# Performance work log

Hardware: AMD Instinct MI355X
Metric: run time of the kernel (lower is better)

Reference implementation:

```python
import jax, jax.numpy as jnp
import numpy as np

HEADS = 6
HSP = 8   # window height (idx=0, split_size=[8,8])
WSP = 8   # window width


def setup_inputs() -> dict:
    key = jax.random.key(0)
    k1, k2, k3 = jax.random.split(key, 3)
    B, C, H, W = 8, 192, 192, 192
    nw = (H // HSP) * (W // WSP)  # 576 windows per image
    kv = jax.random.normal(k1, (2, B, C, H, W), dtype=jnp.float32)
    q = jax.random.normal(k2, (B, C, H, W), dtype=jnp.float32)
    mask = jax.random.normal(k3, (nw, HSP * WSP, HSP * WSP), dtype=jnp.float32)
    return {"kv": kv, "q": q, "mask": mask}


def _vid2win(x, u, v):
    # 'b (d c) (u h) (v w) -> (b u v) d (h w) c'
    B, C, H, W = x.shape
    c = C // HEADS
    hsp, wsp = H // u, W // v
    x = x.reshape(B, HEADS, c, u, hsp, v, wsp)
    x = x.transpose(0, 3, 5, 1, 4, 6, 2)  # B,u,v,d,h,w,c
    return x.reshape(B * u * v, HEADS, hsp * wsp, c)


def reference(kv, q, mask):
    k, v = kv[0], kv[1]
    B, C, H, W = k.shape
    u, w_ = H // HSP, W // WSP
    c = C // HEADS
    scale = c ** (-0.5)
    N = HSP * WSP

    qw = _vid2win(q, u, w_)  # (B*u*w, heads, N, c)
    kw = _vid2win(k, u, w_)
    vw = _vid2win(v, u, w_)

    attn = jnp.einsum('wdnc,wdmc->wdnm', qw, kw) * scale  # (B*u*w, heads, N, N)
    # mask add: 'b (u v) d h w' + mask[None, :, None]
    attn = attn.reshape(B, u * w_, HEADS, N, N) + mask[None, :, None]
    attn = jax.nn.softmax(attn, axis=-1).reshape(B * u * w_, HEADS, N, N)

    x = jnp.einsum('wdnm,wdmc->wdnc', attn, vw)  # (B*u*w, heads, N, c)
    # '(b u v) d (h w) c -> b (d c) (u h) (v w)'
    x = x.reshape(B, u, w_, HEADS, HSP, WSP, c)
    x = x.transpose(0, 3, 6, 1, 4, 2, 5)  # B,d,c,u,h,v,w
    return x.reshape(B, C, H, W)
```

## Files before the change

### kernel.cpp

```cpp
#include <hip/hip_runtime.h>

#define HW_    36864
#define WID_   192
#define CHW_   7077888
#define VOFF_  56623104
#define SCALE_ 0.17677669529663687f

typedef short short8 __attribute__((ext_vector_type(8)));
typedef float f32x4 __attribute__((ext_vector_type(4)));

union Frag { short8 s; unsigned u[4]; };

__device__ __forceinline__ unsigned f2bf_u(float f) {
  union { float f; unsigned u; } x; x.f = f;
  return (x.u + 0x8000u) >> 16;
}
__device__ __forceinline__ unsigned pack_bf(float lo, float hi) {
  union { float f; unsigned u; } a, b; a.f = lo; b.f = hi;
  return ((a.u + 0x8000u) >> 16) | (((b.u + 0x8000u) & 0xFFFF0000u));
}

extern "C" __global__ __launch_bounds__(256, 3)
void win_attn(const float* __restrict__ kv, const float* __restrict__ q,
              const float* __restrict__ mask, float* __restrict__ out) {
  const int tid  = threadIdx.x;
  const int wid  = tid >> 6;
  const int lane = tid & 63;
  const int task = blockIdx.x * 4 + wid;
  const int d    = task % 6;
  const int widx = task / 6;
  const int b    = widx / 576;
  const int uv   = widx % 576;
  const int ui   = uv / 24;
  const int vi   = uv % 24;
  const int base = b * CHW_ + d * (32 * HW_) + ui * (8 * WID_) + vi * 8;

  const float* qg = q  + base;
  const float* kg = kv + base;
  const float* vg = kv + VOFF_ + base;
  const float* mg = mask + uv * 4096;
  float*       og = out + base;

  __shared__ unsigned smem[4][3232];
  unsigned* qsd = smem[wid];
  unsigned* ksd = qsd + 1088;
  unsigned* vtd = qsd + 2176;
  unsigned short* Ps = (unsigned short*)qsd;
  unsigned* Pd = qsd;

  {
    const int n  = lane;
    const int ro = ((n >> 3) * WID_) + (n & 7);
    #pragma unroll
    for (int c2 = 0; c2 < 16; ++c2) {
      const int ch = c2 * 2;
      const float q0 = qg[ch * HW_ + ro];
      const float q1 = qg[(ch + 1) * HW_ + ro];
      const float k0 = kg[ch * HW_ + ro];
      const float k1 = kg[(ch + 1) * HW_ + ro];
      qsd[n * 17 + c2] = pack_bf(q0, q1);
      ksd[n * 17 + c2] = pack_bf(k0, k1);
    }
  }
  {
    const int half = lane >> 5;
    const int m0   = (lane & 31) * 2;
    const int ro   = ((m0 >> 3) * WID_) + (m0 & 7);
    #pragma unroll
    for (int c2 = 0; c2 < 16; ++c2) {
      const int ch = c2 * 2 + half;
      const float2 f2 = *reinterpret_cast<const float2*>(vg + ch * HW_ + ro);
      vtd[ch * 33 + (m0 >> 1)] = pack_bf(f2.x, f2.y);
    }
  }
  __syncthreads();

  const int quad = lane >> 4;
  const int l15  = lane & 15;

  Frag qf[4], kf[4];
  #pragma unroll
  for (int t = 0; t < 4; ++t) {
    const int ad = (t * 16 + l15) * 17 + quad * 4;
    #pragma unroll
    for (int r = 0; r < 4; ++r) { qf[t].u[r] = qsd[ad + r]; kf[t].u[r] = ksd[ad + r]; }
  }

  f32x4 acc[4][4];
  #pragma unroll
  for (int tn = 0; tn < 4; ++tn)
    #pragma unroll
    for (int tm = 0; tm < 4; ++tm) {
      f32x4 z = {0.f, 0.f, 0.f, 0.f};
      acc[tn][tm] = __builtin_amdgcn_mfma_f32_16x16x32_bf16(qf[tn].s, kf[tm].s, z, 0, 0, 0);
    }

  #pragma unroll
  for (int tn = 0; tn < 4; ++tn) {
    #pragma unroll
    for (int r = 0; r < 4; ++r) {
      const int row = tn * 16 + quad * 4 + r;
      const float* mrow = mg + row * 64 + l15;
      const float e0 = __expf(fmaf(acc[tn][0][r], SCALE_, mrow[0]));
      const float e1 = __expf(fmaf(acc[tn][1][r], SCALE_, mrow[16]));
      const float e2 = __expf(fmaf(acc[tn][2][r], SCALE_, mrow[32]));
      const float e3 = __expf(fmaf(acc[tn][3][r], SCALE_, mrow[48]));
      float s = (e0 + e1) + (e2 + e3);
      s += __shfl_xor(s, 1);
      s += __shfl_xor(s, 2);
      s += __shfl_xor(s, 4);
      s += __shfl_xor(s, 8);
      const float rv = __fdividef(1.0f, s);
      const int pb = row * 66 + l15;
      Ps[pb]      = (unsigned short)f2bf_u(e0 * rv);
      Ps[pb + 16] = (unsigned short)f2bf_u(e1 * rv);
      Ps[pb + 32] = (unsigned short)f2bf_u(e2 * rv);
      Ps[pb + 48] = (unsigned short)f2bf_u(e3 * rv);
    }
  }
  __syncthreads();

  Frag va[2][2], pf[4][2];
  #pragma unroll
  for (int ct = 0; ct < 2; ++ct)
    #pragma unroll
    for (int kk = 0; kk < 2; ++kk) {
      const int ad = (ct * 16 + l15) * 33 + kk * 16 + quad * 4;
      #pragma unroll
      for (int r = 0; r < 4; ++r) va[ct][kk].u[r] = vtd[ad + r];
    }
  #pragma unroll
  for (int nt = 0; nt < 4; ++nt)
    #pragma unroll
    for (int kk = 0; kk < 2; ++kk) {
      const int ad = (nt * 16 + l15) * 33 + kk * 16 + quad * 4;
      #pragma unroll
      for (int r = 0; r < 4; ++r) pf[nt][kk].u[r] = Pd[ad + r];
    }

  #pragma unroll
  for (int ct = 0; ct < 2; ++ct)
    #pragma unroll
    for (int nt = 0; nt < 4; ++nt) {
      f32x4 z = {0.f, 0.f, 0.f, 0.f};
      f32x4 o = __builtin_amdgcn_mfma_f32_16x16x32_bf16(va[ct][0].s, pf[nt][0].s, z, 0, 0, 0);
      o       = __builtin_amdgcn_mfma_f32_16x16x32_bf16(va[ct][1].s, pf[nt][1].s, o, 0, 0, 0);
      const int n  = nt * 16 + l15;
      const int so = ((n >> 3) * WID_) + (n & 7);
      #pragma unroll
      for (int r = 0; r < 4; ++r) {
        const int ch = ct * 16 + quad * 4 + r;
        og[ch * HW_ + so] = o[r];
      }
    }
}

extern "C" void kernel_launch(void* const* d_in, const int* in_sizes, int n_in,
                              void* d_out, int out_size, void* d_ws, size_t ws_size,
                              hipStream_t stream) {
  const float* kv   = (const float*)d_in[0];
  const float* q    = (const float*)d_in[1];
  const float* mask = (const float*)d_in[2];
  win_attn<<<dim3(6912), dim3(256), 0, stream>>>(kv, q, mask, (float*)d_out);
}
```

Baseline: 1.015 ms.

## Load Q/K/V fragments directly from global, defer softmax normalization, remap blocks

Drops the LDS staging of Q, K and V: each lane now loads its MFMA fragment straight from global memory (V as float4 vectors), which removes a shared-memory round trip and both __syncthreads. The unnormalized exponentials are written to LDS, and the row reciprocal is applied to the PV output, which also lets the output be stored as f32x4 vectors after the operands are swapped. Blocks are remapped so that four adjacent windows of one (batch, head) sit in one block, shared memory shrinks, and the occupancy hint rises to 4. The direct loads are less coalesced per instruction, and rounding the unnormalized exponentials to bf16 before normalization slightly changes numerics.

After: 889.6 us. -12.4%, faster.

```diff
diff --git a/kernel.cpp b/kernel.cpp
--- a/kernel.cpp
+++ b/kernel.cpp
@@ -17,22 +17,24 @@
 }
 __device__ __forceinline__ unsigned pack_bf(float lo, float hi) {
   union { float f; unsigned u; } a, b; a.f = lo; b.f = hi;
-  return ((a.u + 0x8000u) >> 16) | (((b.u + 0x8000u) & 0xFFFF0000u));
+  return ((a.u + 0x8000u) >> 16) | ((b.u + 0x8000u) & 0xFFFF0000u);
 }
 
-extern "C" __global__ __launch_bounds__(256, 3)
+extern "C" __global__ __launch_bounds__(256, 4)
 void win_attn(const float* __restrict__ kv, const float* __restrict__ q,
               const float* __restrict__ mask, float* __restrict__ out) {
   const int tid  = threadIdx.x;
   const int wid  = tid >> 6;
   const int lane = tid & 63;
-  const int task = blockIdx.x * 4 + wid;
-  const int d    = task % 6;
-  const int widx = task / 6;
-  const int b    = widx / 576;
-  const int uv   = widx % 576;
-  const int ui   = uv / 24;
-  const int vi   = uv % 24;
+  const int bid = blockIdx.x;
+  const int bd  = bid % 48;
+  const int b   = bd / 6;
+  const int d   = bd % 6;
+  const int grp = bid / 48;
+  const int ui  = grp / 6;
+  const int vig = grp % 6;
+  const int vi  = vig * 4 + wid;
+  const int uv  = ui * 24 + vi;
   const int base = b * CHW_ + d * (32 * HW_) + ui * (8 * WID_) + vi * 8;
 
   const float* qg = q  + base;
@@ -41,39 +43,9 @@
   const float* mg = mask + uv * 4096;
   float*       og = out + base;
 
-  __shared__ unsigned smem[4][3232];
-  unsigned* qsd = smem[wid];
-  unsigned* ksd = qsd + 1088;
-  unsigned* vtd = qsd + 2176;
-  unsigned short* Ps = (unsigned short*)qsd;
-  unsigned* Pd = qsd;
-
-  {
-    const int n  = lane;
-    const int ro = ((n >> 3) * WID_) + (n & 7);
-    #pragma unroll
-    for (int c2 = 0; c2 < 16; ++c2) {
-      const int ch = c2 * 2;
-      const float q0 = qg[ch * HW_ + ro];
-      const float q1 = qg[(ch + 1) * HW_ + ro];
-      const float k0 = kg[ch * HW_ + ro];
-      const float k1 = kg[(ch + 1) * HW_ + ro];
-      qsd[n * 17 + c2] = pack_bf(q0, q1);
-      ksd[n * 17 + c2] = pack_bf(k0, k1);
-    }
-  }
-  {
-    const int half = lane >> 5;
-    const int m0   = (lane & 31) * 2;
-    const int ro   = ((m0 >> 3) * WID_) + (m0 & 7);
-    #pragma unroll
-    for (int c2 = 0; c2 < 16; ++c2) {
-      const int ch = c2 * 2 + half;
-      const float2 f2 = *reinterpret_cast<const float2*>(vg + ch * HW_ + ro);
-      vtd[ch * 33 + (m0 >> 1)] = pack_bf(f2.x, f2.y);
-    }
-  }
-  __syncthreads();
+  __shared__ unsigned smem[4][2112];
+  unsigned* Pd = smem[wid];
+  unsigned short* Ps = (unsigned short*)Pd;
 
   const int quad = lane >> 4;
   const int l15  = lane & 15;
@@ -81,54 +53,67 @@
   Frag qf[4], kf[4];
   #pragma unroll
   for (int t = 0; t < 4; ++t) {
-    const int ad = (t * 16 + l15) * 17 + quad * 4;
+    const int n  = t * 16 + l15;
+    const int ro = ((n >> 3) * WID_) + (n & 7);
+    const float* qp = qg + quad * (8 * HW_) + ro;
+    const float* kp = kg + quad * (8 * HW_) + ro;
+    float qv[8], kw[8];
     #pragma unroll
-    for (int r = 0; r < 4; ++r) { qf[t].u[r] = qsd[ad + r]; kf[t].u[r] = ksd[ad + r]; }
+    for (int j = 0; j < 8; ++j) { qv[j] = qp[j * HW_]; kw[j] = kp[j * HW_]; }
+    #pragma unroll
+    for (int r = 0; r < 4; ++r) {
+      qf[t].u[r] = pack_bf(qv[2 * r], qv[2 * r + 1]);
+      kf[t].u[r] = pack_bf(kw[2 * r], kw[2 * r + 1]);
+    }
   }
 
-  f32x4 acc[4][4];
+  float rv[4][4];
   #pragma unroll
-  for (int tn = 0; tn < 4; ++tn)
+  for (int tn = 0; tn < 4; ++tn) {
+    f32x4 acc[4];
     #pragma unroll
     for (int tm = 0; tm < 4; ++tm) {
       f32x4 z = {0.f, 0.f, 0.f, 0.f};
-      acc[tn][tm] = __builtin_amdgcn_mfma_f32_16x16x32_bf16(qf[tn].s, kf[tm].s, z, 0, 0, 0);
+      acc[tm] = __builtin_amdgcn_mfma_f32_16x16x32_bf16(qf[tn].s, kf[tm].s, z, 0, 0, 0);
     }
-
-  #pragma unroll
-  for (int tn = 0; tn < 4; ++tn) {
     #pragma unroll
     for (int r = 0; r < 4; ++r) {
       const int row = tn * 16 + quad * 4 + r;
       const float* mrow = mg + row * 64 + l15;
-      const float e0 = __expf(fmaf(acc[tn][0][r], SCALE_, mrow[0]));
-      const float e1 = __expf(fmaf(acc[tn][1][r], SCALE_, mrow[16]));
-      const float e2 = __expf(fmaf(acc[tn][2][r], SCALE_, mrow[32]));
-      const float e3 = __expf(fmaf(acc[tn][3][r], SCALE_, mrow[48]));
+      const float e0 = __expf(fmaf(acc[0][r], SCALE_, mrow[0]));
+      const float e1 = __expf(fmaf(acc[1][r], SCALE_, mrow[16]));
+      const float e2 = __expf(fmaf(acc[2][r], SCALE_, mrow[32]));
+      const float e3 = __expf(fmaf(acc[3][r], SCALE_, mrow[48]));
+      const int pb = row * 66 + l15;
+      Ps[pb]      = (unsigned short)f2bf_u(e0);
+      Ps[pb + 16] = (unsigned short)f2bf_u(e1);
+      Ps[pb + 32] = (unsigned short)f2bf_u(e2);
+      Ps[pb + 48] = (unsigned short)f2bf_u(e3);
       float s = (e0 + e1) + (e2 + e3);
       s += __shfl_xor(s, 1);
       s += __shfl_xor(s, 2);
       s += __shfl_xor(s, 4);
       s += __shfl_xor(s, 8);
-      const float rv = __fdividef(1.0f, s);
-      const int pb = row * 66 + l15;
-      Ps[pb]      = (unsigned short)f2bf_u(e0 * rv);
-      Ps[pb + 16] = (unsigned short)f2bf_u(e1 * rv);
-      Ps[pb + 32] = (unsigned short)f2bf_u(e2 * rv);
-      Ps[pb + 48] = (unsigned short)f2bf_u(e3 * rv);
+      rv[tn][r] = __fdividef(1.0f, s);
     }
   }
-  __syncthreads();
 
-  Frag va[2][2], pf[4][2];
+  Frag va[2][2];
   #pragma unroll
   for (int ct = 0; ct < 2; ++ct)
     #pragma unroll
     for (int kk = 0; kk < 2; ++kk) {
-      const int ad = (ct * 16 + l15) * 33 + kk * 16 + quad * 4;
-      #pragma unroll
-      for (int r = 0; r < 4; ++r) va[ct][kk].u[r] = vtd[ad + r];
+      const int ch = ct * 16 + l15;
+      const int mr = kk * 4 + quad;
+      const float4 a = *reinterpret_cast<const float4*>(vg + ch * HW_ + mr * WID_);
+      const float4 c = *reinterpret_cast<const float4*>(vg + ch * HW_ + mr * WID_ + 4);
+      va[ct][kk].u[0] = pack_bf(a.x, a.y);
+      va[ct][kk].u[1] = pack_bf(a.z, a.w);
+      va[ct][kk].u[2] = pack_bf(c.x, c.y);
+      va[ct][kk].u[3] = pack_bf(c.z, c.w);
     }
+
+  Frag pf[4][2];
   #pragma unroll
   for (int nt = 0; nt < 4; ++nt)
     #pragma unroll
@@ -143,15 +128,14 @@
     #pragma unroll
     for (int nt = 0; nt < 4; ++nt) {
       f32x4 z = {0.f, 0.f, 0.f, 0.f};
-      f32x4 o = __builtin_amdgcn_mfma_f32_16x16x32_bf16(va[ct][0].s, pf[nt][0].s, z, 0, 0, 0);
-      o       = __builtin_amdgcn_mfma_f32_16x16x32_bf16(va[ct][1].s, pf[nt][1].s, o, 0, 0, 0);
-      const int n  = nt * 16 + l15;
-      const int so = ((n >> 3) * WID_) + (n & 7);
+      f32x4 o = __builtin_amdgcn_mfma_f32_16x16x32_bf16(pf[nt][0].s, va[ct][0].s, z, 0, 0, 0);
+      o       = __builtin_amdgcn_mfma_f32_16x16x32_bf16(pf[nt][1].s, va[ct][1].s, o, 0, 0, 0);
       #pragma unroll
-      for (int r = 0; r < 4; ++r) {
-        const int ch = ct * 16 + quad * 4 + r;
-        og[ch * HW_ + so] = o[r];
-      }
+      for (int r = 0; r < 4; ++r) o[r] *= rv[nt][r];
+      const int n0 = nt * 16 + quad * 4;
+      const int so = ((n0 >> 3) * WID_) + (n0 & 7);
+      const int ch = ct * 16 + l15;
+      *reinterpret_cast<f32x4*>(og + ch * HW_ + so) = o;
     }
 }
 
```
